# Kernel tuning notes

Hardware: AMD Instinct MI355X
Metric: run time of the kernel (lower is better)

The kernel has to match this reference:

```python
import jax, jax.numpy as jnp
import numpy as np
import math

INF = 1e12  # constant.INFINITY_NUMBER in the original repo
B, T, D = 64, 512, 1024  # D = 2 * rnn_hidden


def _lin(k, fan_in, fan_out):
    k1, k2 = jax.random.split(k)
    w = jax.random.normal(k1, (fan_in, fan_out), jnp.float32) / np.float32(np.sqrt(fan_in))
    b = jax.random.normal(k2, (fan_out,), jnp.float32) * 0.01
    return w, b


def setup_inputs() -> dict:
    key = jax.random.key(0)
    ks = jax.random.split(key, 12)
    gcn_inputs = jax.random.normal(ks[0], (B, T, D), jnp.float32)
    subj_pos = jax.random.randint(ks[1], (B, T), 0, 8)  # zeros mark the subject span
    obj_pos = jax.random.randint(ks[2], (B, T), 0, 8)
    masks = jax.random.randint(ks[3], (B, T), 0, 2)
    Wq, bq = _lin(ks[4], 2 * D, D)
    Wc, bc = _lin(ks[5], 2 * D, D)
    Wk, bk = _lin(ks[6], D, 1)
    Wm, bm = _lin(ks[7], 3 * D, D)
    WK, bK = _lin(ks[8], D, D)
    WQ, bQ = _lin(ks[9], D, D)
    WV, bV = _lin(ks[10], D, D)
    return dict(gcn_inputs=gcn_inputs, subj_pos=subj_pos, obj_pos=obj_pos, masks=masks,
                Wq=Wq, bq=bq, Wc=Wc, bc=bc, Wk=Wk, bk=bk, Wm=Wm, bm=bm,
                WK=WK, bK=bK, WQ=WQ, bQ=bQ, WV=WV, bV=bV)


def _pool_max(h, mask):
    # mask: True = masked out
    return jnp.max(jnp.where(mask, jnp.float32(-INF), h), axis=1)


def reference(gcn_inputs, subj_pos, obj_pos, masks,
              Wq, bq, Wc, bc, Wk, bk, Wm, bm, WK, bK, WQ, bQ, WV, bV):
    b, t, d = gcn_inputs.shape
    scale = np.float32(1.0 / math.sqrt(d))

    subj_mask = (subj_pos != 0)[:, :, None]  # .eq(0).eq(0)
    subj_out = _pool_max(gcn_inputs, subj_mask)            # [B, D]
    obj_out = _pool_max(gcn_inputs, subj_mask)             # faithful: original also uses subj_mask here
    subj_obj = jnp.concatenate([subj_out, obj_out], axis=1)  # [B, 2D]

    c0 = jnp.zeros((b, d), gcn_inputs.dtype)
    q = jax.nn.relu(subj_obj @ Wq + bq)                    # [B, D]
    tvec = jax.nn.relu(jnp.concatenate([q, c0], axis=1) @ Wc + bc)  # [B, D]
    k = jax.nn.softmax((tvec[:, None, :] * gcn_inputs) @ Wk + bk, axis=1)  # [B, T, 1]
    c = jnp.sum(k * gcn_inputs, axis=1)                    # [B, D]
    m = jax.nn.relu(jnp.concatenate([c, subj_obj], axis=1) @ Wm + bm)[:, None, :]  # [B, 1, D]

    key_h = gcn_inputs @ WK + bK
    query_h = gcn_inputs @ WQ + bQ
    value_h = gcn_inputs @ WV + bV
    scores = jnp.einsum('btd,bsd->bts', key_h, query_h)    # key.bmm(query^T): [B, T, T]

    # att branch: softmax first, THEN scale (faithful to the original quirk)
    att = jax.nn.softmax(scores, axis=2) * scale
    eye = jnp.eye(t, dtype=bool)[None]
    att = jnp.where(eye, jnp.float32(0.0), att).sum(axis=2)  # [B, T]

    # output branch: scale inside softmax
    probs = jax.nn.softmax(scores * scale, axis=2)
    output = m * jnp.einsum('bts,bsd->btd', probs, value_h)  # gated attention output [B, T, D]

    return output, masks[:, :, None], gcn_inputs, att
```

## Files before the change

kernel.cpp:

```cpp
#include <hip/hip_runtime.h>
#include <hip/hip_bf16.h>

#define B_ 64
#define T_ 512
#define D_ 1024
#define NCH 8
#define TCH 64
#define PSTRIDE 12

#define OUT0_OFF 0u
#define OUT1_OFF 33554432u
#define OUT2_OFF 33587200u
#define OUT3_OFF 67141632u

typedef __attribute__((ext_vector_type(8))) short short8;
typedef __attribute__((ext_vector_type(4))) short short4v;
typedef __attribute__((ext_vector_type(4))) float f32x4;

__device__ __forceinline__ short bf16_of(float x) {
    __hip_bfloat16 h = __float2bfloat16(x);
    return *reinterpret_cast<short*>(&h);
}

__device__ __forceinline__ void gload16(const void* g, void* l) {
    __builtin_amdgcn_global_load_lds(
        (__attribute__((address_space(1))) void*)(g),
        (__attribute__((address_space(3))) void*)(l), 16, 0, 0);
}

__global__ __launch_bounds__(256) void pool_part(const float* __restrict__ gcn,
                                                 const int* __restrict__ subj_pos,
                                                 float* __restrict__ part) {
    __shared__ int keep[TCH];
    int d = threadIdx.x * 4;
    int ch = blockIdx.y, b = blockIdx.z;
    if (threadIdx.x < TCH) keep[threadIdx.x] = (subj_pos[b * T_ + ch * TCH + threadIdx.x] == 0);
    __syncthreads();
    const float* gb = gcn + ((size_t)b * T_ + ch * TCH) * D_ + d;
    f32x4 mx = {-1e12f, -1e12f, -1e12f, -1e12f};
    #pragma unroll 4
    for (int i = 0; i < TCH; i++) {
        f32x4 v = *(const f32x4*)(gb + (size_t)i * D_);
        if (keep[i]) {
            mx[0] = fmaxf(mx[0], v[0]);
            mx[1] = fmaxf(mx[1], v[1]);
            mx[2] = fmaxf(mx[2], v[2]);
            mx[3] = fmaxf(mx[3], v[3]);
        }
    }
    *(f32x4*)(part + ((size_t)b * PSTRIDE + ch) * D_ + d) = mx;
}

__global__ __launch_bounds__(256) void pool_red(const float* __restrict__ part,
                                                float* __restrict__ subj) {
    int d = threadIdx.x * 4;
    int b = blockIdx.y;
    f32x4 mx = {-1e12f, -1e12f, -1e12f, -1e12f};
    #pragma unroll
    for (int ch = 0; ch < NCH; ch++) {
        f32x4 v = *(const f32x4*)(part + ((size_t)b * PSTRIDE + ch) * D_ + d);
        mx[0] = fmaxf(mx[0], v[0]);
        mx[1] = fmaxf(mx[1], v[1]);
        mx[2] = fmaxf(mx[2], v[2]);
        mx[3] = fmaxf(mx[3], v[3]);
    }
    *(f32x4*)(subj + (size_t)b * D_ + d) = mx;
}

__global__ __launch_bounds__(256) void mv_part(const float* __restrict__ x0,
                                               const float* __restrict__ x1,
                                               const float* __restrict__ W,
                                               float* __restrict__ part) {
    __shared__ float xs[256];
    int j = threadIdx.x * 4;
    int ch = blockIdx.y, b = blockIdx.z;
    int gi = ch * 256 + threadIdx.x;
    xs[threadIdx.x] = (gi < D_) ? x0[(size_t)b * D_ + gi]
                                : x1[(size_t)b * D_ + ((gi - D_) & (D_ - 1))];
    __syncthreads();
    const float* Wp = W + (size_t)ch * 256 * D_ + j;
    f32x4 a0 = {}, a1 = {};
    #pragma unroll 4
    for (int i = 0; i < 256; i += 2) {
        f32x4 w0 = *(const f32x4*)(Wp + (size_t)i * D_);
        f32x4 w1 = *(const f32x4*)(Wp + (size_t)(i + 1) * D_);
        a0 += xs[i] * w0;
        a1 += xs[i + 1] * w1;
    }
    *(f32x4*)(part + ((size_t)b * PSTRIDE + ch) * D_ + j) = a0 + a1;
}

__global__ __launch_bounds__(256) void mv_red(const float* __restrict__ part,
                                              const float* __restrict__ bias,
                                              float* __restrict__ y, int nch) {
    int j = threadIdx.x * 4;
    int b = blockIdx.y;
    f32x4 acc = *(const f32x4*)(bias + j);
    for (int ch = 0; ch < nch; ch++)
        acc += *(const f32x4*)(part + ((size_t)b * PSTRIDE + ch) * D_ + j);
    #pragma unroll
    for (int q = 0; q < 4; q++) acc[q] = fmaxf(acc[q], 0.f);
    *(f32x4*)(y + (size_t)b * D_ + j) = acc;
}

__global__ __launch_bounds__(256) void vecs_kernel(const float* __restrict__ WKm,
                                                   const float* __restrict__ WQm,
                                                   const float* __restrict__ bKv,
                                                   const float* __restrict__ bQv,
                                                   float* __restrict__ u,
                                                   float* __restrict__ w,
                                                   float* __restrict__ alpha) {
    int tid = threadIdx.x, wave = tid >> 6, lane = tid & 63;
    int row = blockIdx.x * 4 + wave;
    float s1 = 0.f, s2 = 0.f;
    for (int c = lane; c < D_; c += 64) {
        s1 += WKm[(size_t)row * D_ + c] * bQv[c];
        s2 += WQm[(size_t)row * D_ + c] * bKv[c];
    }
    #pragma unroll
    for (int off = 32; off; off >>= 1) {
        s1 += __shfl_xor(s1, off);
        s2 += __shfl_xor(s2, off);
    }
    if (lane == 0) { u[row] = s1; w[row] = s2; }
    if (blockIdx.x == 0 && wave == 0) {
        float a = 0.f;
        for (int c = lane; c < D_; c += 64) a += bKv[c] * bQv[c];
        #pragma unroll
        for (int off = 32; off; off >>= 1) a += __shfl_xor(a, off);
        if (lane == 0) alpha[0] = a;
    }
}

__global__ __launch_bounds__(256) void att_dots(const float* __restrict__ gcn,
                                                const float* __restrict__ u,
                                                const float* __restrict__ w,
                                                const float* __restrict__ tv,
                                                const float* __restrict__ Wk,
                                                const float* __restrict__ alpha,
                                                const float* __restrict__ bk,
                                                float* __restrict__ Gu,
                                                float* __restrict__ Gw,
                                                float* __restrict__ lg) {
    __shared__ float su[D_], sw[D_], s2[D_];
    int tid = threadIdx.x, wave = tid >> 6, lane = tid & 63;
    size_t row0 = (size_t)blockIdx.x * 4;
    int b = (int)(row0 >> 9);
    for (int c = tid; c < D_; c += 256) {
        su[c] = u[c];
        sw[c] = w[c];
        s2[c] = tv[(size_t)b * D_ + c] * Wk[c];
    }
    __syncthreads();
    size_t row = row0 + wave;
    const float* g = gcn + row * D_;
    float d1 = 0.f, d2 = 0.f, d3 = 0.f;
    #pragma unroll
    for (int it = 0; it < 4; it++) {
        int c = lane * 4 + it * 256;
        f32x4 gv = *(const f32x4*)(g + c);
        f32x4 uu = *(const f32x4*)(su + c);
        f32x4 ww = *(const f32x4*)(sw + c);
        f32x4 kk = *(const f32x4*)(s2 + c);
        #pragma unroll
        for (int q = 0; q < 4; q++) {
            d1 += gv[q] * uu[q];
            d2 += gv[q] * ww[q];
            d3 += gv[q] * kk[q];
        }
    }
    #pragma unroll
    for (int off = 32; off; off >>= 1) {
        d1 += __shfl_xor(d1, off);
        d2 += __shfl_xor(d2, off);
        d3 += __shfl_xor(d3, off);
    }
    if (lane == 0) {
        Gu[row] = d1 + alpha[0];
        Gw[row] = d2;
        lg[row] = d3 + bk[0];
    }
}

__global__ __launch_bounds__(256) void ksoftmax_kernel(float* __restrict__ lg) {
    __shared__ float red[4];
    int b = blockIdx.x, tid = threadIdx.x;
    int wave = tid >> 6, lane = tid & 63;
    float* L = lg + (size_t)b * T_;
    float v0 = L[tid], v1 = L[tid + 256];
    float mx = fmaxf(v0, v1);
    #pragma unroll
    for (int off = 32; off; off >>= 1) mx = fmaxf(mx, __shfl_xor(mx, off));
    if (lane == 0) red[wave] = mx;
    __syncthreads();
    mx = fmaxf(fmaxf(red[0], red[1]), fmaxf(red[2], red[3]));
    __syncthreads();
    float e0 = expf(v0 - mx), e1 = expf(v1 - mx);
    float zs = e0 + e1;
    #pragma unroll
    for (int off = 32; off; off >>= 1) zs += __shfl_xor(zs, off);
    if (lane == 0) red[wave] = zs;
    __syncthreads();
    float invZ = 1.f / (red[0] + red[1] + red[2] + red[3]);
    L[tid] = e0 * invZ;
    L[tid + 256] = e1 * invZ;
}

__global__ __launch_bounds__(256) void csum_part(const float* __restrict__ gcn,
                                                 const float* __restrict__ k,
                                                 float* __restrict__ part) {
    __shared__ float kv[TCH];
    int d = threadIdx.x * 4;
    int ch = blockIdx.y, b = blockIdx.z;
    if (threadIdx.x < TCH) kv[threadIdx.x] = k[(size_t)b * T_ + ch * TCH + threadIdx.x];
    __syncthreads();
    const float* gb = gcn + ((size_t)b * T_ + ch * TCH) * D_ + d;
    f32x4 acc = {};
    #pragma unroll 4
    for (int i = 0; i < TCH; i++) acc += kv[i] * *(const f32x4*)(gb + (size_t)i * D_);
    *(f32x4*)(part + ((size_t)b * PSTRIDE + ch) * D_ + d) = acc;
}

__global__ __launch_bounds__(256) void csum_reduce(const float* __restrict__ part,
                                                   float* __restrict__ cbuf) {
    int d = threadIdx.x * 4;
    int b = blockIdx.y;
    f32x4 acc = {};
    #pragma unroll
    for (int ch = 0; ch < NCH; ch++)
        acc += *(const f32x4*)(part + ((size_t)b * PSTRIDE + ch) * D_ + d);
    *(f32x4*)(cbuf + (size_t)b * D_ + d) = acc;
}

__global__ __launch_bounds__(256) void cast_kernel(const float* __restrict__ in,
                                                   short* __restrict__ out, size_t n8) {
    size_t i = (size_t)blockIdx.x * 256 + threadIdx.x;
    size_t stride = (size_t)gridDim.x * 256;
    for (; i < n8; i += stride) {
        f32x4 v0 = ((const f32x4*)in)[2 * i];
        f32x4 v1 = ((const f32x4*)in)[2 * i + 1];
        short8 o;
        #pragma unroll
        for (int j = 0; j < 4; j++) {
            o[j] = bf16_of(v0[j]);
            o[4 + j] = bf16_of(v1[j]);
        }
        ((short8*)out)[i] = o;
    }
}

__global__ __launch_bounds__(256) void prep_kernel(const float* __restrict__ in,
                                                   short* __restrict__ gs,
                                                   short* __restrict__ gt,
                                                   float* __restrict__ o2) {
    __shared__ float tile[32][33];
    int z = blockIdx.z;
    in += (size_t)z * T_ * D_;
    gs += (size_t)z * T_ * D_;
    gt += (size_t)z * D_ * T_;
    o2 += (size_t)z * T_ * D_;
    int c0 = blockIdx.x * 32, r0 = blockIdx.y * 32;
    int tx = threadIdx.x & 7, ty = threadIdx.x >> 3;
    {
        size_t idx = (size_t)(r0 + ty) * D_ + c0 + tx * 4;
        f32x4 v = *(const f32x4*)(in + idx);
        *(f32x4*)(o2 + idx) = v;
        short4v s;
        #pragma unroll
        for (int q = 0; q < 4; q++) {
            s[q] = bf16_of(v[q]);
            tile[ty][tx * 4 + q] = v[q];
        }
        *(short4v*)(gs + idx) = s;
    }
    __syncthreads();
    int tx2 = threadIdx.x & 31, ty2 = threadIdx.x >> 5;
    #pragma unroll
    for (int i = 0; i < 4; i++) {
        int c = ty2 + i * 8;
        gt[(size_t)(c0 + c) * T_ + r0 + tx2] = bf16_of(tile[tx2][c]);
    }
}

__global__ __launch_bounds__(256) void transpose_kernel(const float* __restrict__ in, size_t sIn,
                                                        short* __restrict__ out, size_t sOut,
                                                        int R, int C) {
    __shared__ float tile[32][33];
    int z = blockIdx.z;
    in += (size_t)z * sIn;
    out += (size_t)z * sOut;
    int c0 = blockIdx.x * 32, r0 = blockIdx.y * 32;
    int tx = threadIdx.x & 31, ty = threadIdx.x >> 5;
    #pragma unroll
    for (int i = 0; i < 4; i++) {
        int r = ty + i * 8;
        tile[r][tx] = in[(size_t)(r0 + r) * C + c0 + tx];
    }
    __syncthreads();
    #pragma unroll
    for (int i = 0; i < 4; i++) {
        int c = ty + i * 8;
        out[(size_t)(c0 + c) * R + r0 + tx] = bf16_of(tile[tx][c]);
    }
}

template <int MODE>
__global__ __launch_bounds__(256) void gemm_nt(
        const short* __restrict__ A, size_t sAz,
        const short* __restrict__ Bt, size_t sBz,
        int K, int ldout,
        float* __restrict__ Cf, short* __restrict__ Cb, size_t sCz,
        const float* __restrict__ e1, const float* __restrict__ e2) {
    __shared__ __align__(16) short As[128 * 64];
    __shared__ __align__(16) short Bs[128 * 64];
    unsigned gx = gridDim.x, gy = gridDim.y;
    unsigned lin = blockIdx.x + gx * (blockIdx.y + gy * blockIdx.z);
    unsigned tot = gx * gy * gridDim.z;
    unsigned swz = (lin & 7u) * (tot >> 3) + (lin >> 3);
    unsigned bx = swz % gx;
    unsigned tmp = swz / gx;
    unsigned by = tmp % gy;
    unsigned bz = tmp / gy;

    int z = bz;
    A += (size_t)z * sAz;
    Bt += (size_t)z * sBz;
    int t = threadIdx.x;
    int lane = t & 63, wave = t >> 6;
    int wr = wave >> 1, wc = wave & 1;
    size_t rowBase = (size_t)bx * 128;
    size_t colBase = (size_t)by * 128;

    int rlo = lane >> 3;
    int src16 = (lane & 7) ^ rlo;
    const short* gA[4];
    const short* gB[4];
    short* lA[4];
    short* lB[4];
    #pragma unroll
    for (int i = 0; i < 4; i++) {
        int ch = wave * 4 + i;
        int row = ch * 8 + rlo;
        gA[i] = A + (rowBase + row) * (size_t)K + src16 * 8;
        gB[i] = Bt + (colBase + row) * (size_t)K + src16 * 8;
        lA[i] = As + ch * 512;
        lB[i] = Bs + ch * 512;
    }

    f32x4 acc[4][4] = {};
    for (int kb = 0; kb < K; kb += 64) {
        __syncthreads();
        #pragma unroll
        for (int i = 0; i < 4; i++) {
            gload16(gA[i] + kb, lA[i]);
            gload16(gB[i] + kb, lB[i]);
        }
        __syncthreads();
        #pragma unroll
        for (int kk = 0; kk < 2; kk++) {
            int ko16 = kk * 4 + (lane >> 4);
            int sw = ko16 ^ (lane & 7);
            short8 af[4], bfr[4];
            #pragma unroll
            for (int i = 0; i < 4; i++) {
                int row = wr * 64 + i * 16 + (lane & 15);
                af[i] = *(const short8*)(As + row * 64 + (sw << 3));
            }
            #pragma unroll
            for (int j = 0; j < 4; j++) {
                int row = wc * 64 + j * 16 + (lane & 15);
                bfr[j] = *(const short8*)(Bs + row * 64 + (sw << 3));
            }
            #pragma unroll
            for (int i = 0; i < 4; i++)
                #pragma unroll
                for (int j = 0; j < 4; j++)
                    acc[i][j] = __builtin_amdgcn_mfma_f32_16x16x32_bf16(af[i], bfr[j], acc[i][j], 0, 0, 0);
        }
    }
    #pragma unroll
    for (int i = 0; i < 4; i++) {
        #pragma unroll
        for (int j = 0; j < 4; j++) {
            #pragma unroll
            for (int r = 0; r < 4; r++) {
                size_t row = rowBase + wr * 64 + i * 16 + (lane >> 4) * 4 + r;
                size_t col = colBase + wc * 64 + j * 16 + (lane & 15);
                float v = acc[i][j][r];
                if (MODE == 0) {
                    Cf[z * sCz + row * ldout + col] = v;
                } else if (MODE == 1) {
                    Cf[z * sCz + row * ldout + col] = v + e1[z * T_ + row] + e2[z * T_ + col];
                } else if (MODE == 2) {
                    Cb[z * sCz + row * ldout + col] = bf16_of(v);
                } else {
                    Cf[z * sCz + row * ldout + col] = (v + e1[col]) * e2[(size_t)z * D_ + col];
                }
            }
        }
    }
}

__global__ __launch_bounds__(256) void softmax_att(const float* __restrict__ S,
                                                   short* __restrict__ probs,
                                                   float* __restrict__ att) {
    const float SCALE = 0.03125f;
    int wave = threadIdx.x >> 6, lane = threadIdx.x & 63;
    int t = blockIdx.x * 4 + wave, z = blockIdx.y;
    const float* row = S + ((size_t)z * T_ + t) * T_;
    short* prow = probs + ((size_t)z * T_ + t) * T_;
    float v[8];
    float mx = -1e30f;
    #pragma unroll
    for (int k = 0; k < 8; k++) {
        v[k] = row[lane + k * 64];
        mx = fmaxf(mx, v[k]);
    }
    #pragma unroll
    for (int off = 32; off; off >>= 1) mx = fmaxf(mx, __shfl_xor(mx, off));
    float z1 = 0.f, z2 = 0.f, dg = 0.f;
    #pragma unroll
    for (int k = 0; k < 8; k++) {
        float x = v[k] - mx;
        float e1 = expf(x);
        float e2 = expf(x * SCALE);
        z1 += e1;
        z2 += e2;
        if (lane + k * 64 == t) dg = e1;
        v[k] = e2;
    }
    #pragma unroll
    for (int off = 32; off; off >>= 1) {
        z1 += __shfl_xor(z1, off);
        z2 += __shfl_xor(z2, off);
        dg += __shfl_xor(dg, off);
    }
    float inv2 = 1.f / z2;
    #pragma unroll
    for (int k = 0; k < 8; k++) prow[lane + k * 64] = bf16_of(v[k] * inv2);
    if (lane == 0) att[z * T_ + t] = SCALE * (1.f - dg / z1);
}

__global__ __launch_bounds__(256) void masks_kernel(const int* __restrict__ masks,
                                                    float* __restrict__ out_masks) {
    int i = blockIdx.x * 256 + threadIdx.x;
    if (i < B_ * T_) out_masks[i] = (float)masks[i];
}

extern "C" void kernel_launch(void* const* d_in, const int* in_sizes, int n_in,
                              void* d_out, int out_size, void* d_ws, size_t ws_size,
                              hipStream_t stream) {
    const float* gcn = (const float*)d_in[0];
    const int* subj_pos = (const int*)d_in[1];
    const int* masks = (const int*)d_in[3];
    const float* Wq = (const float*)d_in[4];
    const float* bq = (const float*)d_in[5];
    const float* Wc = (const float*)d_in[6];
    const float* bc = (const float*)d_in[7];
    const float* Wk = (const float*)d_in[8];
    const float* bk = (const float*)d_in[9];
    const float* Wm = (const float*)d_in[10];
    const float* bm = (const float*)d_in[11];
    const float* WK = (const float*)d_in[12];
    const float* bK = (const float*)d_in[13];
    const float* WQ = (const float*)d_in[14];
    const float* bQ = (const float*)d_in[15];
    const float* WV = (const float*)d_in[16];
    const float* bV = (const float*)d_in[17];

    float* out = (float*)d_out;

    char* p = (char*)d_ws;
    auto alloc = [&](size_t bytes) {
        char* r = p;
        p += (bytes + 255) & ~(size_t)255;
        return r;
    };
    float* subj = (float*)alloc(B_ * D_ * 4);
    float* qv   = (float*)alloc(B_ * D_ * 4);
    float* tv   = (float*)alloc(B_ * D_ * 4);
    float* cb   = (float*)alloc(B_ * D_ * 4);
    float* mb   = (float*)alloc(B_ * D_ * 4);
    float* u    = (float*)alloc(D_ * 4);
    float* w    = (float*)alloc(D_ * 4);
    float* alph = (float*)alloc(256);
    float* Gu   = (float*)alloc(B_ * T_ * 4);
    float* Gw   = (float*)alloc(B_ * T_ * 4);
    float* lg   = (float*)alloc(B_ * T_ * 4);
    float* part = (float*)alloc((size_t)B_ * PSTRIDE * D_ * 4);
    float* Pt   = (float*)alloc((size_t)D_ * D_ * 4);
    short* WKb  = (short*)alloc((size_t)D_ * D_ * 2);
    short* WQb  = (short*)alloc((size_t)D_ * D_ * 2);
    short* Ptb  = (short*)alloc((size_t)D_ * D_ * 2);
    short* WVt  = (short*)alloc((size_t)D_ * D_ * 2);

    size_t fixedBytes = (size_t)(p - (char*)d_ws);
    const size_t perBatch = (size_t)T_ * D_ * 2
                          + (size_t)T_ * D_ * 2
                          + (size_t)D_ * T_ * 2
                          + (size_t)T_ * T_ * 4
                          + (size_t)T_ * T_ * 2
                          + (size_t)T_ * D_ * 2;
    int nc = 64;
    while (nc > 1 && fixedBytes + (size_t)nc * perBatch + 4096 > ws_size) nc >>= 1;

    short* Gs_c    = (short*)alloc((size_t)nc * T_ * D_ * 2);
    short* Ys_c    = (short*)alloc((size_t)nc * T_ * D_ * 2);
    short* Gt_c    = (short*)alloc((size_t)nc * D_ * T_ * 2);
    float* S_c     = (float*)alloc((size_t)nc * T_ * T_ * 4);
    short* probs_c = (short*)alloc((size_t)nc * T_ * T_ * 2);
    short* Zs_c    = (short*)alloc((size_t)nc * T_ * D_ * 2);

    pool_part<<<dim3(1, NCH, B_), 256, 0, stream>>>(gcn, subj_pos, part);
    pool_red<<<dim3(1, B_), 256, 0, stream>>>(part, subj);
    mv_part<<<dim3(1, 8, B_), 256, 0, stream>>>(subj, subj, Wq, part);
    mv_red<<<dim3(1, B_), 256, 0, stream>>>(part, bq, qv, 8);
    mv_part<<<dim3(1, 4, B_), 256, 0, stream>>>(qv, qv, Wc, part);
    mv_red<<<dim3(1, B_), 256, 0, stream>>>(part, bc, tv, 4);
    vecs_kernel<<<D_ / 4, 256, 0, stream>>>(WK, WQ, bK, bQ, u, w, alph);
    att_dots<<<B_ * T_ / 4, 256, 0, stream>>>(gcn, u, w, tv, Wk, alph, bk, Gu, Gw, lg);
    ksoftmax_kernel<<<B_, 256, 0, stream>>>(lg);
    csum_part<<<dim3(1, NCH, B_), 256, 0, stream>>>(gcn, lg, part);
    csum_reduce<<<dim3(1, B_), 256, 0, stream>>>(part, cb);
    mv_part<<<dim3(1, 12, B_), 256, 0, stream>>>(cb, subj, Wm, part);
    mv_red<<<dim3(1, B_), 256, 0, stream>>>(part, bm, mb, 12);

    cast_kernel<<<512, 256, 0, stream>>>(WK, WKb, (size_t)D_ * D_ / 8);
    cast_kernel<<<512, 256, 0, stream>>>(WQ, WQb, (size_t)D_ * D_ / 8);
    gemm_nt<0><<<dim3(8, 8, 1), 256, 0, stream>>>(WQb, 0, WKb, 0, D_, D_,
                                                  Pt, nullptr, 0, nullptr, nullptr);
    cast_kernel<<<512, 256, 0, stream>>>(Pt, Ptb, (size_t)D_ * D_ / 8);
    transpose_kernel<<<dim3(32, 32, 1), 256, 0, stream>>>(WV, 0, WVt, 0, D_, D_);

    for (int b0 = 0; b0 < B_; b0 += nc) {
        const float* Gc = gcn + (size_t)b0 * T_ * D_;
        prep_kernel<<<dim3(D_ / 32, T_ / 32, nc), 256, 0, stream>>>(
            Gc, Gs_c, Gt_c, out + OUT2_OFF + (size_t)b0 * T_ * D_);
        gemm_nt<2><<<dim3(nc * T_ / 128, D_ / 128, 1), 256, 0, stream>>>(
            Gs_c, 0, Ptb, 0, D_, D_, nullptr, Ys_c, 0, nullptr, nullptr);
        gemm_nt<1><<<dim3(T_ / 128, T_ / 128, nc), 256, 0, stream>>>(
            Ys_c, (size_t)T_ * D_, Gs_c, (size_t)T_ * D_, D_, T_,
            S_c, nullptr, (size_t)T_ * T_, Gu + (size_t)b0 * T_, Gw + (size_t)b0 * T_);
        softmax_att<<<dim3(T_ / 4, nc), 256, 0, stream>>>(S_c, probs_c, out + OUT3_OFF + (size_t)b0 * T_);
        gemm_nt<2><<<dim3(T_ / 128, D_ / 128, nc), 256, 0, stream>>>(
            probs_c, (size_t)T_ * T_, Gt_c, (size_t)D_ * T_, T_, D_,
            nullptr, Zs_c, (size_t)T_ * D_, nullptr, nullptr);
        gemm_nt<3><<<dim3(T_ / 128, D_ / 128, nc), 256, 0, stream>>>(
            Zs_c, (size_t)T_ * D_, WVt, 0, D_, D_,
            out + OUT0_OFF + (size_t)b0 * T_ * D_, nullptr, (size_t)T_ * D_,
            bV, mb + (size_t)b0 * D_);
    }

    masks_kernel<<<(B_ * T_ + 255) / 256, 256, 0, stream>>>(masks, out + OUT1_OFF);
}
```

Measured before the change: 631.3 us.

## Replace small fp32 matvec layers with bf16 MFMA GEMMs and fused epilogues

The three small dense layers (Wq, Wc, Wm) previously ran as per-batch fp32 matrix-vector partial/reduce kernels that re-read each weight matrix for every batch row. They now batch all 64 rows into one bf16 GEMM per layer using the existing MFMA gemm_nt kernel, with new epilogue modes for bias+ReLU that emit fp32 or bf16. The pooling and context-sum reductions write bf16 activation buffers directly. This removes the redundant weight traffic and the separate reduction launches, but adds weight transposes each call, runs only 8 blocks per GEMM with a long K loop, and lowers these layers to bf16 precision.

```diff
diff --git a/kernel.cpp b/kernel.cpp
--- a/kernel.cpp
+++ b/kernel.cpp
@@ -52,7 +52,9 @@
 }
 
 __global__ __launch_bounds__(256) void pool_red(const float* __restrict__ part,
-                                                float* __restrict__ subj) {
+                                                float* __restrict__ subj,
+                                                short* __restrict__ aq,
+                                                short* __restrict__ am) {
     int d = threadIdx.x * 4;
     int b = blockIdx.y;
     f32x4 mx = {-1e12f, -1e12f, -1e12f, -1e12f};
@@ -65,42 +67,13 @@
         mx[3] = fmaxf(mx[3], v[3]);
     }
     *(f32x4*)(subj + (size_t)b * D_ + d) = mx;
-}
-
-__global__ __launch_bounds__(256) void mv_part(const float* __restrict__ x0,
-                                               const float* __restrict__ x1,
-                                               const float* __restrict__ W,
-                                               float* __restrict__ part) {
-    __shared__ float xs[256];
-    int j = threadIdx.x * 4;
-    int ch = blockIdx.y, b = blockIdx.z;
-    int gi = ch * 256 + threadIdx.x;
-    xs[threadIdx.x] = (gi < D_) ? x0[(size_t)b * D_ + gi]
-                                : x1[(size_t)b * D_ + ((gi - D_) & (D_ - 1))];
-    __syncthreads();
-    const float* Wp = W + (size_t)ch * 256 * D_ + j;
-    f32x4 a0 = {}, a1 = {};
-    #pragma unroll 4
-    for (int i = 0; i < 256; i += 2) {
-        f32x4 w0 = *(const f32x4*)(Wp + (size_t)i * D_);
-        f32x4 w1 = *(const f32x4*)(Wp + (size_t)(i + 1) * D_);
-        a0 += xs[i] * w0;
-        a1 += xs[i + 1] * w1;
-    }
-    *(f32x4*)(part + ((size_t)b * PSTRIDE + ch) * D_ + j) = a0 + a1;
-}
-
-__global__ __launch_bounds__(256) void mv_red(const float* __restrict__ part,
-                                              const float* __restrict__ bias,
-                                              float* __restrict__ y, int nch) {
-    int j = threadIdx.x * 4;
-    int b = blockIdx.y;
-    f32x4 acc = *(const f32x4*)(bias + j);
-    for (int ch = 0; ch < nch; ch++)
-        acc += *(const f32x4*)(part + ((size_t)b * PSTRIDE + ch) * D_ + j);
-    #pragma unroll
-    for (int q = 0; q < 4; q++) acc[q] = fmaxf(acc[q], 0.f);
-    *(f32x4*)(y + (size_t)b * D_ + j) = acc;
+    short4v s;
+    #pragma unroll
+    for (int q = 0; q < 4; q++) s[q] = bf16_of(mx[q]);
+    *(short4v*)(aq + (size_t)b * 2048 + d) = s;
+    *(short4v*)(aq + (size_t)b * 2048 + 1024 + d) = s;
+    *(short4v*)(am + (size_t)b * 3072 + 1024 + d) = s;
+    *(short4v*)(am + (size_t)b * 3072 + 2048 + d) = s;
 }
 
 __global__ __launch_bounds__(256) void vecs_kernel(const float* __restrict__ WKm,
@@ -222,7 +195,8 @@
 }
 
 __global__ __launch_bounds__(256) void csum_reduce(const float* __restrict__ part,
-                                                   float* __restrict__ cbuf) {
+                                                   float* __restrict__ cbuf,
+                                                   short* __restrict__ am) {
     int d = threadIdx.x * 4;
     int b = blockIdx.y;
     f32x4 acc = {};
@@ -230,6 +204,10 @@
     for (int ch = 0; ch < NCH; ch++)
         acc += *(const f32x4*)(part + ((size_t)b * PSTRIDE + ch) * D_ + d);
     *(f32x4*)(cbuf + (size_t)b * D_ + d) = acc;
+    short4v s;
+    #pragma unroll
+    for (int q = 0; q < 4; q++) s[q] = bf16_of(acc[q]);
+    *(short4v*)(am + (size_t)b * 3072 + d) = s;
 }
 
 __global__ __launch_bounds__(256) void cast_kernel(const float* __restrict__ in,
@@ -310,7 +288,7 @@
         const short* __restrict__ Bt, size_t sBz,
         int K, int ldout,
         float* __restrict__ Cf, short* __restrict__ Cb, size_t sCz,
-        const float* __restrict__ e1, const float* __restrict__ e2) {
+        const float* __restrict__ e1, const float* __restrict__ e2, int mvalid) {
     __shared__ __align__(16) short As[128 * 64];
     __shared__ __align__(16) short Bs[128 * 64];
     unsigned gx = gridDim.x, gy = gridDim.y;
@@ -393,8 +371,12 @@
                     Cf[z * sCz + row * ldout + col] = v + e1[z * T_ + row] + e2[z * T_ + col];
                 } else if (MODE == 2) {
                     Cb[z * sCz + row * ldout + col] = bf16_of(v);
+                } else if (MODE == 3) {
+                    Cf[z * sCz + row * ldout + col] = (v + e1[col]) * e2[(size_t)z * D_ + col];
+                } else if (MODE == 4) {
+                    if ((int)row < mvalid) Cf[z * sCz + row * ldout + col] = fmaxf(v + e1[col], 0.f);
                 } else {
-                    Cf[z * sCz + row * ldout + col] = (v + e1[col]) * e2[(size_t)z * D_ + col];
+                    if ((int)row < mvalid) Cb[z * sCz + row * ldout + col] = bf16_of(fmaxf(v + e1[col], 0.f));
                 }
             }
         }
@@ -469,6 +451,7 @@
     const float* bV = (const float*)d_in[17];
 
     float* out = (float*)d_out;
+    const int BIGM = 1 << 30;
 
     char* p = (char*)d_ws;
     auto alloc = [&](size_t bytes) {
@@ -477,7 +460,6 @@
         return r;
     };
     float* subj = (float*)alloc(B_ * D_ * 4);
-    float* qv   = (float*)alloc(B_ * D_ * 4);
     float* tv   = (float*)alloc(B_ * D_ * 4);
     float* cb   = (float*)alloc(B_ * D_ * 4);
     float* mb   = (float*)alloc(B_ * D_ * 4);
@@ -493,6 +475,12 @@
     short* WQb  = (short*)alloc((size_t)D_ * D_ * 2);
     short* Ptb  = (short*)alloc((size_t)D_ * D_ * 2);
     short* WVt  = (short*)alloc((size_t)D_ * D_ * 2);
+    short* Wqt  = (short*)alloc((size_t)D_ * 2 * D_ * 2);
+    short* Wct  = (short*)alloc((size_t)D_ * D_ * 2);
+    short* Wmt  = (short*)alloc((size_t)D_ * 3 * D_ * 2);
+    short* Aq   = (short*)alloc((size_t)128 * 2048 * 2);
+    short* Atv  = (short*)alloc((size_t)128 * 1024 * 2);
+    short* Am   = (short*)alloc((size_t)128 * 3072 * 2);
 
     size_t fixedBytes = (size_t)(p - (char*)d_ws);
     const size_t perBatch = (size_t)T_ * D_ * 2
@@ -511,24 +499,28 @@
     short* probs_c = (short*)alloc((size_t)nc * T_ * T_ * 2);
     short* Zs_c    = (short*)alloc((size_t)nc * T_ * D_ * 2);
 
+    transpose_kernel<<<dim3(D_ / 32, 2 * D_ / 32, 1), 256, 0, stream>>>(Wq, 0, Wqt, 0, 2 * D_, D_);
+    transpose_kernel<<<dim3(D_ / 32, D_ / 32, 1), 256, 0, stream>>>(Wc, 0, Wct, 0, D_, D_);
+    transpose_kernel<<<dim3(D_ / 32, 3 * D_ / 32, 1), 256, 0, stream>>>(Wm, 0, Wmt, 0, 3 * D_, D_);
+
     pool_part<<<dim3(1, NCH, B_), 256, 0, stream>>>(gcn, subj_pos, part);
-    pool_red<<<dim3(1, B_), 256, 0, stream>>>(part, subj);
-    mv_part<<<dim3(1, 8, B_), 256, 0, stream>>>(subj, subj, Wq, part);
-    mv_red<<<dim3(1, B_), 256, 0, stream>>>(part, bq, qv, 8);
-    mv_part<<<dim3(1, 4, B_), 256, 0, stream>>>(qv, qv, Wc, part);
-    mv_red<<<dim3(1, B_), 256, 0, stream>>>(part, bc, tv, 4);
+    pool_red<<<dim3(1, B_), 256, 0, stream>>>(part, subj, Aq, Am);
+    gemm_nt<5><<<dim3(1, 8, 1), 256, 0, stream>>>(Aq, 0, Wqt, 0, 2 * D_, D_,
+                                                  nullptr, Atv, 0, bq, nullptr, B_);
+    gemm_nt<4><<<dim3(1, 8, 1), 256, 0, stream>>>(Atv, 0, Wct, 0, D_, D_,
+                                                  tv, nullptr, 0, bc, nullptr, B_);
     vecs_kernel<<<D_ / 4, 256, 0, stream>>>(WK, WQ, bK, bQ, u, w, alph);
     att_dots<<<B_ * T_ / 4, 256, 0, stream>>>(gcn, u, w, tv, Wk, alph, bk, Gu, Gw, lg);
     ksoftmax_kernel<<<B_, 256, 0, stream>>>(lg);
     csum_part<<<dim3(1, NCH, B_), 256, 0, stream>>>(gcn, lg, part);
-    csum_reduce<<<dim3(1, B_), 256, 0, stream>>>(part, cb);
-    mv_part<<<dim3(1, 12, B_), 256, 0, stream>>>(cb, subj, Wm, part);
-    mv_red<<<dim3(1, B_), 256, 0, stream>>>(part, bm, mb, 12);
+    csum_reduce<<<dim3(1, B_), 256, 0, stream>>>(part, cb, Am);
+    gemm_nt<4><<<dim3(1, 8, 1), 256, 0, stream>>>(Am, 0, Wmt, 0, 3 * D_, D_,
+                                                  mb, nullptr, 0, bm, nullptr, B_);
 
     cast_kernel<<<512, 256, 0, stream>>>(WK, WKb, (size_t)D_ * D_ / 8);
     cast_kernel<<<512, 256, 0, stream>>>(WQ, WQb, (size_t)D_ * D_ / 8);
     gemm_nt<0><<<dim3(8, 8, 1), 256, 0, stream>>>(WQb, 0, WKb, 0, D_, D_,
-                                                  Pt, nullptr, 0, nullptr, nullptr);
+                                                  Pt, nullptr, 0, nullptr, nullptr, BIGM);
     cast_kernel<<<512, 256, 0, stream>>>(Pt, Ptb, (size_t)D_ * D_ / 8);
     transpose_kernel<<<dim3(32, 32, 1), 256, 0, stream>>>(WV, 0, WVt, 0, D_, D_);
 
@@ -537,18 +529,18 @@
         prep_kernel<<<dim3(D_ / 32, T_ / 32, nc), 256, 0, stream>>>(
             Gc, Gs_c, Gt_c, out + OUT2_OFF + (size_t)b0 * T_ * D_);
         gemm_nt<2><<<dim3(nc * T_ / 128, D_ / 128, 1), 256, 0, stream>>>(
-            Gs_c, 0, Ptb, 0, D_, D_, nullptr, Ys_c, 0, nullptr, nullptr);
+            Gs_c, 0, Ptb, 0, D_, D_, nullptr, Ys_c, 0, nullptr, nullptr, BIGM);
         gemm_nt<1><<<dim3(T_ / 128, T_ / 128, nc), 256, 0, stream>>>(
             Ys_c, (size_t)T_ * D_, Gs_c, (size_t)T_ * D_, D_, T_,
-            S_c, nullptr, (size_t)T_ * T_, Gu + (size_t)b0 * T_, Gw + (size_t)b0 * T_);
+            S_c, nullptr, (size_t)T_ * T_, Gu + (size_t)b0 * T_, Gw + (size_t)b0 * T_, BIGM);
         softmax_att<<<dim3(T_ / 4, nc), 256, 0, stream>>>(S_c, probs_c, out + OUT3_OFF + (size_t)b0 * T_);
         gemm_nt<2><<<dim3(T_ / 128, D_ / 128, nc), 256, 0, stream>>>(
             probs_c, (size_t)T_ * T_, Gt_c, (size_t)D_ * T_, T_, D_,
-            nullptr, Zs_c, (size_t)T_ * D_, nullptr, nullptr);
+            nullptr, Zs_c, (size_t)T_ * D_, nullptr, nullptr, BIGM);
         gemm_nt<3><<<dim3(T_ / 128, D_ / 128, nc), 256, 0, stream>>>(
             Zs_c, (size_t)T_ * D_, WVt, 0, D_, D_,
             out + OUT0_OFF + (size_t)b0 * T_ * D_, nullptr, (size_t)T_ * D_,
-            bV, mb + (size_t)b0 * D_);
+            bV, mb + (size_t)b0 * D_, BIGM);
     }
 
     masks_kernel<<<(B_ * T_ + 255) / 256, 256, 0, stream>>>(masks, out + OUT1_OFF);
```

Measured after the change: 700.5 us. +11.0%, slower.

## Batch small matvecs into tiled GEMM sharing weight tiles across the batch

Applied to the files above, without the earlier changes.

Replaces the per-batch matrix-vector kernels, which each streamed the full weight matrix once per batch row, with a tiled small GEMM. Each block stages a 128x64 weight tile and the matching input slice for all 64 batch rows in shared memory, so each weight is read once instead of 64 times. Partial sums over K chunks go to a new workspace buffer and a reduction kernel adds bias and applies ReLU. This costs more workspace and a larger reduction pass, and the shared-memory column reads may hit bank conflicts.

```diff
diff --git a/kernel.cpp b/kernel.cpp
--- a/kernel.cpp
+++ b/kernel.cpp
@@ -7,6 +7,7 @@
 #define NCH 8
 #define TCH 64
 #define PSTRIDE 12
+#define MVKC 128
 
 #define OUT0_OFF 0u
 #define OUT1_OFF 33554432u
@@ -67,37 +68,51 @@
     *(f32x4*)(subj + (size_t)b * D_ + d) = mx;
 }
 
-__global__ __launch_bounds__(256) void mv_part(const float* __restrict__ x0,
-                                               const float* __restrict__ x1,
-                                               const float* __restrict__ W,
-                                               float* __restrict__ part) {
-    __shared__ float xs[256];
-    int j = threadIdx.x * 4;
-    int ch = blockIdx.y, b = blockIdx.z;
-    int gi = ch * 256 + threadIdx.x;
-    xs[threadIdx.x] = (gi < D_) ? x0[(size_t)b * D_ + gi]
-                                : x1[(size_t)b * D_ + ((gi - D_) & (D_ - 1))];
-    __syncthreads();
-    const float* Wp = W + (size_t)ch * 256 * D_ + j;
-    f32x4 a0 = {}, a1 = {};
-    #pragma unroll 4
-    for (int i = 0; i < 256; i += 2) {
-        f32x4 w0 = *(const f32x4*)(Wp + (size_t)i * D_);
-        f32x4 w1 = *(const f32x4*)(Wp + (size_t)(i + 1) * D_);
-        a0 += xs[i] * w0;
-        a1 += xs[i + 1] * w1;
-    }
-    *(f32x4*)(part + ((size_t)b * PSTRIDE + ch) * D_ + j) = a0 + a1;
-}
-
-__global__ __launch_bounds__(256) void mv_red(const float* __restrict__ part,
-                                              const float* __restrict__ bias,
-                                              float* __restrict__ y, int nch) {
+__global__ __launch_bounds__(256) void mvg_part(const float* __restrict__ x0,
+                                                const float* __restrict__ x1,
+                                                const float* __restrict__ W,
+                                                float* __restrict__ pmv) {
+    __shared__ float xs[MVKC][64];
+    __shared__ float ws[MVKC][64];
+    int n0 = blockIdx.x * 64;
+    int k0 = blockIdx.y * MVKC;
+    for (int i = threadIdx.x; i < MVKC * 64; i += 256) {
+        int k = i >> 6, b = i & 63;
+        int kg = k0 + k;
+        xs[k][b] = (kg < D_) ? x0[(size_t)b * D_ + kg]
+                             : x1[(size_t)b * D_ + ((kg - D_) & (D_ - 1))];
+    }
+    for (int i = threadIdx.x; i < MVKC * 16; i += 256) {
+        int r = i >> 4, c4 = (i & 15) * 4;
+        *(f32x4*)&ws[r][c4] = *(const f32x4*)(W + (size_t)(k0 + r) * D_ + n0 + c4);
+    }
+    __syncthreads();
+    int n = threadIdx.x & 63;
+    int bg = (threadIdx.x >> 6) * 16;
+    f32x4 acc[4] = {};
+    for (int k = 0; k < MVKC; k++) {
+        float wv = ws[k][n];
+        #pragma unroll
+        for (int g = 0; g < 4; g++) {
+            f32x4 xv = *(const f32x4*)&xs[k][bg + g * 4];
+            acc[g] += xv * wv;
+        }
+    }
+    #pragma unroll
+    for (int g = 0; g < 4; g++)
+        #pragma unroll
+        for (int q = 0; q < 4; q++)
+            pmv[((size_t)blockIdx.y * 64 + bg + g * 4 + q) * D_ + n0 + n] = acc[g][q];
+}
+
+__global__ __launch_bounds__(256) void mvg_red(const float* __restrict__ pmv,
+                                               const float* __restrict__ bias,
+                                               float* __restrict__ y, int nkch) {
     int j = threadIdx.x * 4;
     int b = blockIdx.y;
     f32x4 acc = *(const f32x4*)(bias + j);
-    for (int ch = 0; ch < nch; ch++)
-        acc += *(const f32x4*)(part + ((size_t)b * PSTRIDE + ch) * D_ + j);
+    for (int kch = 0; kch < nkch; kch++)
+        acc += *(const f32x4*)(pmv + ((size_t)kch * 64 + b) * D_ + j);
     #pragma unroll
     for (int q = 0; q < 4; q++) acc[q] = fmaxf(acc[q], 0.f);
     *(f32x4*)(y + (size_t)b * D_ + j) = acc;
@@ -488,6 +503,7 @@
     float* Gw   = (float*)alloc(B_ * T_ * 4);
     float* lg   = (float*)alloc(B_ * T_ * 4);
     float* part = (float*)alloc((size_t)B_ * PSTRIDE * D_ * 4);
+    float* pmv  = (float*)alloc((size_t)24 * 64 * D_ * 4);
     float* Pt   = (float*)alloc((size_t)D_ * D_ * 4);
     short* WKb  = (short*)alloc((size_t)D_ * D_ * 2);
     short* WQb  = (short*)alloc((size_t)D_ * D_ * 2);
@@ -513,17 +529,17 @@
 
     pool_part<<<dim3(1, NCH, B_), 256, 0, stream>>>(gcn, subj_pos, part);
     pool_red<<<dim3(1, B_), 256, 0, stream>>>(part, subj);
-    mv_part<<<dim3(1, 8, B_), 256, 0, stream>>>(subj, subj, Wq, part);
-    mv_red<<<dim3(1, B_), 256, 0, stream>>>(part, bq, qv, 8);
-    mv_part<<<dim3(1, 4, B_), 256, 0, stream>>>(qv, qv, Wc, part);
-    mv_red<<<dim3(1, B_), 256, 0, stream>>>(part, bc, tv, 4);
+    mvg_part<<<dim3(D_ / 64, 16), 256, 0, stream>>>(subj, subj, Wq, pmv);
+    mvg_red<<<dim3(1, B_), 256, 0, stream>>>(pmv, bq, qv, 16);
+    mvg_part<<<dim3(D_ / 64, 8), 256, 0, stream>>>(qv, qv, Wc, pmv);
+    mvg_red<<<dim3(1, B_), 256, 0, stream>>>(pmv, bc, tv, 8);
     vecs_kernel<<<D_ / 4, 256, 0, stream>>>(WK, WQ, bK, bQ, u, w, alph);
     att_dots<<<B_ * T_ / 4, 256, 0, stream>>>(gcn, u, w, tv, Wk, alph, bk, Gu, Gw, lg);
     ksoftmax_kernel<<<B_, 256, 0, stream>>>(lg);
     csum_part<<<dim3(1, NCH, B_), 256, 0, stream>>>(gcn, lg, part);
     csum_reduce<<<dim3(1, B_), 256, 0, stream>>>(part, cb);
-    mv_part<<<dim3(1, 12, B_), 256, 0, stream>>>(cb, subj, Wm, part);
-    mv_red<<<dim3(1, B_), 256, 0, stream>>>(part, bm, mb, 12);
+    mvg_part<<<dim3(D_ / 64, 24), 256, 0, stream>>>(cb, subj, Wm, pmv);
+    mvg_red<<<dim3(1, B_), 256, 0, stream>>>(pmv, bm, mb, 24);
 
     cast_kernel<<<512, 256, 0, stream>>>(WK, WKb, (size_t)D_ * D_ / 8);
     cast_kernel<<<512, 256, 0, stream>>>(WQ, WQb, (size_t)D_ * D_ / 8);
```

Measured after the change: 608.8 us. 1.04x faster.
